# Kernel tuning notes

Hardware: AMD Instinct MI355X
Metric: run time of the kernel (lower is better)

Reference implementation:

```python
import jax, jax.numpy as jnp
import numpy as np

N_NODES = 50000
N_EDGES = 800000
DIM = 96
N_LAYERS = 3
N_GRAPHS = 128
OUT_DIM = 10


def setup_inputs() -> dict:
    key = jax.random.key(0)
    ks = jax.random.split(key, 9)
    s = 1.0 / np.sqrt(DIM)
    return {
        "x": jax.random.normal(ks[0], (N_NODES, DIM), dtype=jnp.float32),
        "edge_index": jax.random.randint(ks[1], (2, N_EDGES), 0, N_NODES, dtype=jnp.int32),
        "batch": jnp.sort(jax.random.randint(ks[2], (N_NODES,), 0, N_GRAPHS, dtype=jnp.int32)),
        "W1": jax.random.normal(ks[3], (N_LAYERS, DIM, DIM), dtype=jnp.float32) * s,
        "W2": jax.random.normal(ks[4], (N_LAYERS, DIM, DIM), dtype=jnp.float32) * s,
        "cw1": jax.random.normal(ks[5], (DIM, DIM), dtype=jnp.float32) * s,
        "cb1": jax.random.normal(ks[6], (DIM,), dtype=jnp.float32) * s,
        "cw2": jax.random.normal(ks[7], (DIM, OUT_DIM), dtype=jnp.float32) * s,
        "cb2": jax.random.normal(ks[8], (OUT_DIM,), dtype=jnp.float32) * s,
    }


def reference(x, edge_index, batch, W1, W2, cw1, cb1, cw2, cb2):
    src, dst = edge_index[0], edge_index[1]
    h = x
    for l in range(N_LAYERS):
        self_part = h @ W1[l]                       # [N, D]
        # transform at node level then gather per edge (same math as per-edge W2(x_j))
        msg = (h @ W2[l])[src]                      # [E, D]
        neighbor_part = jax.ops.segment_sum(msg, dst, num_segments=N_NODES)
        h = jax.nn.relu(self_part + neighbor_part)
    graph_emb = jax.ops.segment_sum(h, batch, num_segments=N_GRAPHS)  # [G, D]
    hidden = jax.nn.relu(graph_emb @ cw1 + cb1)
    return hidden @ cw2 + cb2                       # [G, OUT_DIM]
```

## Files before the change

kernel.cpp:

```cpp
#include <hip/hip_runtime.h>

#define N_NODES   50000
#define N_EDGES   800000
#define DIM       96
#define N_GRAPHS  128
#define OUT_DIM   10
#define NPAD      50048
#define CAP       64
#define NBINS     391
#define BINCAP    4096
#define P1_BLOCKS 256
#define EPB       (N_EDGES / P1_BLOCKS)
#define LPAD      104

#define CAST_NB   ((N_NODES * 12 + 255) / 256)
#define CONV_NB   ((3 * DIM * 2 * DIM + 255) / 256)
#define ZERO_NB   ((NBINS * 16 + 255) / 256)

typedef __attribute__((ext_vector_type(8))) short          short8;
typedef __attribute__((ext_vector_type(8))) unsigned short u16x8;
typedef __attribute__((ext_vector_type(4))) float          f32x4;

__device__ __forceinline__ float b2f(unsigned short u) {
    union { unsigned int i; float f; } v; v.i = ((unsigned int)u) << 16; return v.f;
}
__device__ __forceinline__ unsigned short f2b(float f) {
    union { float f; unsigned int i; } v; v.f = f;
    unsigned int u = v.i;
    return (unsigned short)((u + 0x7fffu + ((u >> 16) & 1u)) >> 16);
}

__global__ __launch_bounds__(256) void prep(const float* __restrict__ x,
                                            const float* __restrict__ W1,
                                            const float* __restrict__ W2,
                                            unsigned short* __restrict__ harr,
                                            unsigned short* __restrict__ Bt,
                                            int* __restrict__ gcur)
{
    const int b = blockIdx.x;
    const int t = threadIdx.x;
    if (b < CAST_NB) {
        const int tid = b * 256 + t;
        if (tid >= N_NODES * 12) return;
        const int node = tid / 12;
        const int c    = (tid - node * 12) * 8;
        const float4 v0 = *(const float4*)(x + (size_t)node * DIM + c);
        const float4 v1 = *(const float4*)(x + (size_t)node * DIM + c + 4);
        u16x8 o;
        o[0] = f2b(v0.x); o[1] = f2b(v0.y); o[2] = f2b(v0.z); o[3] = f2b(v0.w);
        o[4] = f2b(v1.x); o[5] = f2b(v1.y); o[6] = f2b(v1.z); o[7] = f2b(v1.w);
        *(u16x8*)(harr + (size_t)node * DIM + c) = o;
    } else if (b < CAST_NB + CONV_NB) {
        const int idx = (b - CAST_NB) * 256 + t;
        if (idx >= 3 * DIM * 2 * DIM) return;
        const int l   = idx / (DIM * 2 * DIM);
        const int rem = idx - l * (DIM * 2 * DIM);
        const int n   = rem / (2 * DIM);
        const int k   = rem - n * (2 * DIM);
        const float v = (k < DIM) ? W1[(size_t)l * DIM * DIM + k * DIM + n]
                                  : W2[(size_t)l * DIM * DIM + (k - DIM) * DIM + n];
        Bt[idx] = f2b(v);
    } else {
        const int i = (b - CAST_NB - CONV_NB) * 256 + t;
        if (i < NBINS * 16) gcur[i] = 0;
    }
}

__global__ __launch_bounds__(256) void pass1_bin(const int* __restrict__ src,
                                                 const int* __restrict__ dst,
                                                 int* __restrict__ gcur,
                                                 int* __restrict__ binned)
{
    __shared__ int hist[NBINS];
    __shared__ int base[NBINS];
    const int t  = threadIdx.x;
    const int e0 = blockIdx.x * EPB;

    for (int b = t; b < NBINS; b += 256) hist[b] = 0;
    __syncthreads();

    for (int e = e0 + t; e < e0 + EPB; e += 256)
        atomicAdd(&hist[dst[e] >> 7], 1);
    __syncthreads();

    for (int b = t; b < NBINS; b += 256) {
        const int c = hist[b];
        base[b] = (c > 0) ? atomicAdd(&gcur[b << 4], c) : 0;
        hist[b] = 0;
    }
    __syncthreads();

    for (int e = e0 + t; e < e0 + EPB; e += 256) {
        const int d   = dst[e];
        const int bin = d >> 7;
        const int pos = base[bin] + atomicAdd(&hist[bin], 1);
        if (pos < BINCAP)
            binned[bin * BINCAP + pos] = ((d & 127) << 16) | src[e];
    }
}

__global__ __launch_bounds__(256) void pass2_scatter(const int* __restrict__ gcur,
                                                     const int* __restrict__ binned,
                                                     int* __restrict__ csrc,
                                                     int* __restrict__ deg)
{
    __shared__ int ncnt[128];
    const int bin = blockIdx.x;
    const int t   = threadIdx.x;
    const int n0  = bin << 7;
    const int cnt = min(gcur[bin << 4], BINCAP);

    if (t < 128) ncnt[t] = 0;
    __syncthreads();

    const int* __restrict__ bb = binned + bin * BINCAP;
    for (int i = t; i < cnt; i += 256) {
        const int v    = bb[i];
        const int dlow = v >> 16;
        const int s    = v & 0xffff;
        const int pos  = atomicAdd(&ncnt[dlow], 1);
        if (pos < CAP) csrc[(size_t)(n0 + dlow) * CAP + pos] = s;
    }
    __syncthreads();

    if (t < 128 && n0 + t < N_NODES) deg[n0 + t] = min(ncnt[t], CAP);
}

__global__ __launch_bounds__(384) void gnn_layer(
    const unsigned short* __restrict__ harr, const int* __restrict__ deg,
    const int* __restrict__ csrc, const unsigned short* __restrict__ Btl,
    unsigned short* __restrict__ hout)
{
    __shared__ unsigned short aggLds[64][LPAD];
    const int t       = threadIdx.x;
    const int rowBase = blockIdx.x * 64;

    {
        const int r    = t / 6;
        const int sub  = t - r * 6;
        const int node = rowBase + r;
        const int off  = sub * 16;

        float a[16];
#pragma unroll
        for (int i = 0; i < 16; i++) a[i] = 0.f;

        if (node < N_NODES) {
            const int d = deg[node];
            const int* __restrict__ bkt = csrc + (size_t)node * CAP;
            const unsigned short* __restrict__ hb = harr + off;

            const int nfull = d & ~3;
            int c = 0;
            for (; c < nfull; c += 4) {
                const int4 s = *(const int4*)(bkt + c);
                const unsigned short* p0 = hb + (size_t)s.x * DIM;
                const unsigned short* p1 = hb + (size_t)s.y * DIM;
                const unsigned short* p2 = hb + (size_t)s.z * DIM;
                const unsigned short* p3 = hb + (size_t)s.w * DIM;
                const u16x8 va0 = *(const u16x8*)(p0), vb0 = *(const u16x8*)(p0 + 8);
                const u16x8 va1 = *(const u16x8*)(p1), vb1 = *(const u16x8*)(p1 + 8);
                const u16x8 va2 = *(const u16x8*)(p2), vb2 = *(const u16x8*)(p2 + 8);
                const u16x8 va3 = *(const u16x8*)(p3), vb3 = *(const u16x8*)(p3 + 8);
#pragma unroll
                for (int i = 0; i < 8; i++) {
                    a[i]     += b2f(va0[i]) + b2f(va1[i]) + b2f(va2[i]) + b2f(va3[i]);
                    a[i + 8] += b2f(vb0[i]) + b2f(vb1[i]) + b2f(vb2[i]) + b2f(vb3[i]);
                }
            }
            for (; c < d; c++) {
                const unsigned short* p0 = hb + (size_t)bkt[c] * DIM;
                const u16x8 va0 = *(const u16x8*)(p0), vb0 = *(const u16x8*)(p0 + 8);
#pragma unroll
                for (int i = 0; i < 8; i++) {
                    a[i]     += b2f(va0[i]);
                    a[i + 8] += b2f(vb0[i]);
                }
            }
        }

        u16x8 o0, o1;
#pragma unroll
        for (int i = 0; i < 8; i++) { o0[i] = f2b(a[i]); o1[i] = f2b(a[i + 8]); }
        *(u16x8*)(&aggLds[r][off])     = o0;
        *(u16x8*)(&aggLds[r][off + 8]) = o1;
    }
    __syncthreads();

    const int lane = t & 63;
    const int w    = t >> 6;
    const int m    = lane & 15;
    const int q    = lane >> 4;

    short8 bfrag[6];
#pragma unroll
    for (int s = 0; s < 6; s++)
        bfrag[s] = *(const short8*)(Btl + (size_t)(w * 16 + m) * (2 * DIM) + s * 32 + q * 8);

#pragma unroll
    for (int r = 0; r < 4; r++) {
        const int rb = rowBase + r * 16;
        f32x4 acc = {0.f, 0.f, 0.f, 0.f};
        const unsigned short* ah = harr + (size_t)(rb + m) * DIM + q * 8;
#pragma unroll
        for (int s = 0; s < 3; s++) {
            const short8 af = *(const short8*)(ah + s * 32);
            acc = __builtin_amdgcn_mfma_f32_16x16x32_bf16(af, bfrag[s], acc, 0, 0, 0);
        }
#pragma unroll
        for (int s = 0; s < 3; s++) {
            const short8 af = *(const short8*)(&aggLds[r * 16 + m][s * 32 + q * 8]);
            acc = __builtin_amdgcn_mfma_f32_16x16x32_bf16(af, bfrag[s + 3], acc, 0, 0, 0);
        }
#pragma unroll
        for (int i = 0; i < 4; i++) {
            const int grow = rb + q * 4 + i;
            if (grow < N_NODES)
                hout[(size_t)grow * DIM + w * 16 + m] = f2b(fmaxf(acc[i], 0.f));
        }
    }
}

__global__ __launch_bounds__(384) void pool_classify(
    const unsigned short* __restrict__ h, const int* __restrict__ batch,
    const float* __restrict__ cw1, const float* __restrict__ cb1,
    const float* __restrict__ cw2, const float* __restrict__ cb2,
    float* __restrict__ out)
{
    const int g = blockIdx.x;
    const int t = threadIdx.x;

    int lo = 0, hi = N_NODES;
    while (lo < hi) { int m = (lo + hi) >> 1; if (batch[m] < g) lo = m + 1; else hi = m; }
    const int start = lo;
    hi = N_NODES;
    while (lo < hi) { int m = (lo + hi) >> 1; if (batch[m] < g + 1) lo = m + 1; else hi = m; }
    const int end = lo;

    __shared__ float part[4][DIM];
    __shared__ float gr[DIM];
    __shared__ float hid[DIM];

    const int col = t % DIM;
    const int ty  = t / DIM;

    float s = 0.f;
    for (int n = start + ty; n < end; n += 4)
        s += b2f(h[(size_t)n * DIM + col]);
    part[ty][col] = s;
    __syncthreads();
    if (ty == 0)
        gr[col] = part[0][col] + part[1][col] + part[2][col] + part[3][col];
    __syncthreads();

    float hsum = 0.f;
    const int k0 = ty * (DIM / 4);
#pragma unroll 4
    for (int k = k0; k < k0 + DIM / 4; k++)
        hsum += gr[k] * cw1[k * DIM + col];
    part[ty][col] = hsum;
    __syncthreads();
    if (ty == 0)
        hid[col] = fmaxf(part[0][col] + part[1][col] + part[2][col] + part[3][col]
                         + cb1[col], 0.f);
    __syncthreads();

    if (t < OUT_DIM) {
        float o = cb2[t];
#pragma unroll 4
        for (int k = 0; k < DIM; k++) o += hid[k] * cw2[k * OUT_DIM + t];
        out[g * OUT_DIM + t] = o;
    }
}

extern "C" void kernel_launch(void* const* d_in, const int* in_sizes, int n_in,
                              void* d_out, int out_size, void* d_ws, size_t ws_size,
                              hipStream_t stream)
{
    const float* x     = (const float*)d_in[0];
    const int*   ei    = (const int*)  d_in[1];
    const int*   batch = (const int*)  d_in[2];
    const float* W1    = (const float*)d_in[3];
    const float* W2    = (const float*)d_in[4];
    const float* cw1   = (const float*)d_in[5];
    const float* cb1   = (const float*)d_in[6];
    const float* cw2   = (const float*)d_in[7];
    const float* cb2   = (const float*)d_in[8];
    float*       out   = (float*)d_out;

    const int* src = ei;
    const int* dst = ei + N_EDGES;

    unsigned short* bufA = (unsigned short*)d_ws;
    unsigned short* bufB = bufA + (size_t)NPAD * DIM;
    unsigned short* Bt   = bufB + (size_t)NPAD * DIM;
    int*   gcur   = (int*)(Bt + 3 * DIM * 2 * DIM);
    int*   binned = gcur + NBINS * 16;
    int*   csrc   = binned + (size_t)NBINS * BINCAP;
    int*   deg    = csrc + (size_t)N_NODES * CAP;

    prep<<<CAST_NB + CONV_NB + ZERO_NB, 256, 0, stream>>>(x, W1, W2, bufA, Bt, gcur);
    pass1_bin<<<P1_BLOCKS, 256, 0, stream>>>(src, dst, gcur, binned);
    pass2_scatter<<<NBINS, 256, 0, stream>>>(gcur, binned, csrc, deg);

    unsigned short* hin  = bufA;
    unsigned short* hout = bufB;
    for (int l = 0; l < 3; l++) {
        gnn_layer<<<NPAD / 64, 384, 0, stream>>>(hin, deg, csrc,
                                                 Bt + (size_t)l * DIM * 2 * DIM, hout);
        unsigned short* tmp = hin; hin = hout; hout = tmp;
    }

    pool_classify<<<N_GRAPHS, 384, 0, stream>>>(hin, batch, cw1, cb1, cw2, cb2, out);
}
```

Before: 267.7 us.

## Reorder nodes by in-degree buckets for load-balanced gnn_layer blocks

Nodes are grouped by degree through a counting bucket sort in pass2_scatter, and a new bucket_prefix kernel computes the bucket offsets. Each gnn_layer block then processes 64 nodes of similar degree, found by binary search over those offsets, instead of 64 consecutive nodes. This aims to cut wavefront divergence and tail imbalance in the gather loop. In exchange it adds a small kernel launch, a per-row binary search and indirection, and the A-tile loads and output stores become scattered rows instead of contiguous ones.

```diff
diff --git a/kernel.cpp b/kernel.cpp
--- a/kernel.cpp
+++ b/kernel.cpp
@@ -12,10 +12,13 @@
 #define P1_BLOCKS 256
 #define EPB       (N_EDGES / P1_BLOCKS)
 #define LPAD      104
+#define NDB       65
+#define PBCAP     8192
 
 #define CAST_NB   ((N_NODES * 12 + 255) / 256)
 #define CONV_NB   ((3 * DIM * 2 * DIM + 255) / 256)
-#define ZERO_NB   ((NBINS * 16 + 255) / 256)
+#define ZERO_CNT  ((NBINS + NDB) * 16)
+#define ZERO_NB   ((ZERO_CNT + 255) / 256)
 
 typedef __attribute__((ext_vector_type(8))) short          short8;
 typedef __attribute__((ext_vector_type(8))) unsigned short u16x8;
@@ -62,7 +65,7 @@
         Bt[idx] = f2b(v);
     } else {
         const int i = (b - CAST_NB - CONV_NB) * 256 + t;
-        if (i < NBINS * 16) gcur[i] = 0;
+        if (i < ZERO_CNT) gcur[i] = 0;
     }
 }
 
@@ -102,7 +105,9 @@
 __global__ __launch_bounds__(256) void pass2_scatter(const int* __restrict__ gcur,
                                                      const int* __restrict__ binned,
                                                      int* __restrict__ csrc,
-                                                     int* __restrict__ deg)
+                                                     int* __restrict__ deg,
+                                                     int* __restrict__ bcnt,
+                                                     int* __restrict__ pbin)
 {
     __shared__ int ncnt[128];
     const int bin = blockIdx.x;
@@ -123,29 +128,64 @@
     }
     __syncthreads();
 
-    if (t < 128 && n0 + t < N_NODES) deg[n0 + t] = min(ncnt[t], CAP);
+    if (t < 128 && n0 + t < N_NODES) {
+        const int n = n0 + t;
+        const int d = min(ncnt[t], CAP);
+        deg[n] = d;
+        const int pos = atomicAdd(&bcnt[d << 4], 1);
+        if (pos < PBCAP) pbin[d * PBCAP + pos] = n;
+    }
+}
+
+__global__ __launch_bounds__(128) void bucket_prefix(const int* __restrict__ bcnt,
+                                                     int* __restrict__ boff)
+{
+    __shared__ int c[NDB];
+    const int t = threadIdx.x;
+    if (t < NDB) c[t] = min(bcnt[t << 4], PBCAP);
+    __syncthreads();
+    if (t == 0) {
+        int acc = 0;
+        for (int b = 0; b < NDB; b++) { boff[b] = acc; acc += c[b]; }
+        boff[NDB] = acc;
+    }
 }
 
 __global__ __launch_bounds__(384) void gnn_layer(
     const unsigned short* __restrict__ harr, const int* __restrict__ deg,
-    const int* __restrict__ csrc, const unsigned short* __restrict__ Btl,
+    const int* __restrict__ csrc, const int* __restrict__ pbin,
+    const int* __restrict__ boff, const unsigned short* __restrict__ Btl,
     unsigned short* __restrict__ hout)
 {
     __shared__ unsigned short aggLds[64][LPAD];
+    __shared__ int boffL[NDB + 1];
+    __shared__ int nodeIds[64];
     const int t       = threadIdx.x;
     const int rowBase = blockIdx.x * 64;
 
+    if (t < NDB + 1) boffL[t] = boff[t];
+    __syncthreads();
+
     {
-        const int r    = t / 6;
-        const int sub  = t - r * 6;
-        const int node = rowBase + r;
-        const int off  = sub * 16;
+        const int r   = t / 6;
+        const int sub = t - r * 6;
+        const int g   = rowBase + r;
+        const int off = sub * 16;
+
+        int node = -1;
+        if (g < N_NODES) {
+            int lo = 0, hi = NDB - 1;
+            while (lo < hi) { int mid = (lo + hi + 1) >> 1;
+                              if (boffL[mid] <= g) lo = mid; else hi = mid - 1; }
+            node = pbin[lo * PBCAP + (g - boffL[lo])];
+        }
+        if (sub == 0) nodeIds[r] = node;
 
         float a[16];
 #pragma unroll
         for (int i = 0; i < 16; i++) a[i] = 0.f;
 
-        if (node < N_NODES) {
+        if (node >= 0) {
             const int d = deg[node];
             const int* __restrict__ bkt = csrc + (size_t)node * CAP;
             const unsigned short* __restrict__ hb = harr + off;
@@ -199,9 +239,9 @@
 
 #pragma unroll
     for (int r = 0; r < 4; r++) {
-        const int rb = rowBase + r * 16;
         f32x4 acc = {0.f, 0.f, 0.f, 0.f};
-        const unsigned short* ah = harr + (size_t)(rb + m) * DIM + q * 8;
+        const int nodeA = nodeIds[r * 16 + m];
+        const unsigned short* ah = harr + (size_t)max(nodeA, 0) * DIM + q * 8;
 #pragma unroll
         for (int s = 0; s < 3; s++) {
             const short8 af = *(const short8*)(ah + s * 32);
@@ -214,9 +254,9 @@
         }
 #pragma unroll
         for (int i = 0; i < 4; i++) {
-            const int grow = rb + q * 4 + i;
-            if (grow < N_NODES)
-                hout[(size_t)grow * DIM + w * 16 + m] = f2b(fmaxf(acc[i], 0.f));
+            const int nodeC = nodeIds[r * 16 + q * 4 + i];
+            if (nodeC >= 0)
+                hout[(size_t)nodeC * DIM + w * 16 + m] = f2b(fmaxf(acc[i], 0.f));
         }
     }
 }
@@ -295,18 +335,22 @@
     unsigned short* bufB = bufA + (size_t)NPAD * DIM;
     unsigned short* Bt   = bufB + (size_t)NPAD * DIM;
     int*   gcur   = (int*)(Bt + 3 * DIM * 2 * DIM);
-    int*   binned = gcur + NBINS * 16;
+    int*   bcnt   = gcur + NBINS * 16;
+    int*   binned = bcnt + NDB * 16;
     int*   csrc   = binned + (size_t)NBINS * BINCAP;
     int*   deg    = csrc + (size_t)N_NODES * CAP;
+    int*   pbin   = deg + N_NODES;
+    int*   boff   = pbin + NDB * PBCAP;
 
     prep<<<CAST_NB + CONV_NB + ZERO_NB, 256, 0, stream>>>(x, W1, W2, bufA, Bt, gcur);
     pass1_bin<<<P1_BLOCKS, 256, 0, stream>>>(src, dst, gcur, binned);
-    pass2_scatter<<<NBINS, 256, 0, stream>>>(gcur, binned, csrc, deg);
+    pass2_scatter<<<NBINS, 256, 0, stream>>>(gcur, binned, csrc, deg, bcnt, pbin);
+    bucket_prefix<<<1, 128, 0, stream>>>(bcnt, boff);
 
     unsigned short* hin  = bufA;
     unsigned short* hout = bufB;
     for (int l = 0; l < 3; l++) {
-        gnn_layer<<<NPAD / 64, 384, 0, stream>>>(hin, deg, csrc,
+        gnn_layer<<<NPAD / 64, 384, 0, stream>>>(hin, deg, csrc, pbin, boff,
                                                  Bt + (size_t)l * DIM * 2 * DIM, hout);
         unsigned short* tmp = hin; hin = hout; hout = tmp;
     }
```

Result: slower. 361.9 us (+35.2%).

## Replace global-atomic edge binning with per-block slices and prefix scan

Applied to the files above, without the earlier changes.

Edge binning now has each of 128 blocks write into its own fixed-size slice per destination bin. Per-slice counts replace the global atomic cursor and its zeroing pass. The scatter pass prefix-scans the slice counts and binary-searches each edge's slice. This removes one histogram pass and the global atomics, but adds a scan and a binary search per edge in pass 2. The fixed slice capacity of 48 may drop edges if a block holds more than 48 edges for one bin. The layer kernel also issues its weight-fragment loads before the aggregation phase so they can overlap it.

```diff
diff --git a/kernel.cpp b/kernel.cpp
--- a/kernel.cpp
+++ b/kernel.cpp
@@ -6,16 +6,15 @@
 #define N_GRAPHS  128
 #define OUT_DIM   10
 #define NPAD      50048
+#define NBINS     391
+#define P1_BLOCKS 128
+#define EPB       (N_EDGES / P1_BLOCKS)
+#define SLICECAP  48
 #define CAP       64
-#define NBINS     391
-#define BINCAP    4096
-#define P1_BLOCKS 256
-#define EPB       (N_EDGES / P1_BLOCKS)
 #define LPAD      104
 
 #define CAST_NB   ((N_NODES * 12 + 255) / 256)
 #define CONV_NB   ((3 * DIM * 2 * DIM + 255) / 256)
-#define ZERO_NB   ((NBINS * 16 + 255) / 256)
 
 typedef __attribute__((ext_vector_type(8))) short          short8;
 typedef __attribute__((ext_vector_type(8))) unsigned short u16x8;
@@ -34,8 +33,7 @@
                                             const float* __restrict__ W1,
                                             const float* __restrict__ W2,
                                             unsigned short* __restrict__ harr,
-                                            unsigned short* __restrict__ Bt,
-                                            int* __restrict__ gcur)
+                                            unsigned short* __restrict__ Bt)
 {
     const int b = blockIdx.x;
     const int t = threadIdx.x;
@@ -50,7 +48,7 @@
         o[0] = f2b(v0.x); o[1] = f2b(v0.y); o[2] = f2b(v0.z); o[3] = f2b(v0.w);
         o[4] = f2b(v1.x); o[5] = f2b(v1.y); o[6] = f2b(v1.z); o[7] = f2b(v1.w);
         *(u16x8*)(harr + (size_t)node * DIM + c) = o;
-    } else if (b < CAST_NB + CONV_NB) {
+    } else {
         const int idx = (b - CAST_NB) * 256 + t;
         if (idx >= 3 * DIM * 2 * DIM) return;
         const int l   = idx / (DIM * 2 * DIM);
@@ -60,62 +58,71 @@
         const float v = (k < DIM) ? W1[(size_t)l * DIM * DIM + k * DIM + n]
                                   : W2[(size_t)l * DIM * DIM + (k - DIM) * DIM + n];
         Bt[idx] = f2b(v);
-    } else {
-        const int i = (b - CAST_NB - CONV_NB) * 256 + t;
-        if (i < NBINS * 16) gcur[i] = 0;
     }
 }
 
 __global__ __launch_bounds__(256) void pass1_bin(const int* __restrict__ src,
                                                  const int* __restrict__ dst,
-                                                 int* __restrict__ gcur,
-                                                 int* __restrict__ binned)
-{
-    __shared__ int hist[NBINS];
-    __shared__ int base[NBINS];
-    const int t  = threadIdx.x;
-    const int e0 = blockIdx.x * EPB;
-
-    for (int b = t; b < NBINS; b += 256) hist[b] = 0;
-    __syncthreads();
-
-    for (int e = e0 + t; e < e0 + EPB; e += 256)
-        atomicAdd(&hist[dst[e] >> 7], 1);
-    __syncthreads();
-
-    for (int b = t; b < NBINS; b += 256) {
-        const int c = hist[b];
-        base[b] = (c > 0) ? atomicAdd(&gcur[b << 4], c) : 0;
-        hist[b] = 0;
-    }
+                                                 int* __restrict__ binned,
+                                                 int* __restrict__ cnt)
+{
+    __shared__ int cur[NBINS];
+    const int t   = threadIdx.x;
+    const int blk = blockIdx.x;
+    const int e0  = blk * EPB;
+
+    for (int b = t; b < NBINS; b += 256) cur[b] = 0;
     __syncthreads();
 
     for (int e = e0 + t; e < e0 + EPB; e += 256) {
         const int d   = dst[e];
         const int bin = d >> 7;
-        const int pos = base[bin] + atomicAdd(&hist[bin], 1);
-        if (pos < BINCAP)
-            binned[bin * BINCAP + pos] = ((d & 127) << 16) | src[e];
-    }
-}
-
-__global__ __launch_bounds__(256) void pass2_scatter(const int* __restrict__ gcur,
+        const int pos = atomicAdd(&cur[bin], 1);
+        if (pos < SLICECAP)
+            binned[((size_t)bin * P1_BLOCKS + blk) * SLICECAP + pos]
+                = ((d & 127) << 16) | src[e];
+    }
+    __syncthreads();
+
+    for (int b = t; b < NBINS; b += 256)
+        cnt[b * P1_BLOCKS + blk] = min(cur[b], SLICECAP);
+}
+
+__global__ __launch_bounds__(256) void pass2_scatter(const int* __restrict__ cnt,
                                                      const int* __restrict__ binned,
                                                      int* __restrict__ csrc,
                                                      int* __restrict__ deg)
 {
+    __shared__ int buf[2][P1_BLOCKS];
+    __shared__ int soff[P1_BLOCKS + 1];
     __shared__ int ncnt[128];
     const int bin = blockIdx.x;
     const int t   = threadIdx.x;
     const int n0  = bin << 7;
-    const int cnt = min(gcur[bin << 4], BINCAP);
-
-    if (t < 128) ncnt[t] = 0;
-    __syncthreads();
-
-    const int* __restrict__ bb = binned + bin * BINCAP;
-    for (int i = t; i < cnt; i += 256) {
-        const int v    = bb[i];
+
+    if (t < P1_BLOCKS) { buf[0][t] = cnt[bin * P1_BLOCKS + t]; ncnt[t] = 0; }
+    __syncthreads();
+
+    int c = 0;
+#pragma unroll
+    for (int off = 1; off < P1_BLOCKS; off <<= 1) {
+        if (t < P1_BLOCKS) {
+            int x = buf[c][t];
+            if (t >= off) x += buf[c][t - off];
+            buf[c ^ 1][t] = x;
+        }
+        __syncthreads();
+        c ^= 1;
+    }
+    if (t < P1_BLOCKS) { soff[t + 1] = buf[c][t]; if (t == 0) soff[0] = 0; }
+    __syncthreads();
+
+    const int Eb = soff[P1_BLOCKS];
+    for (int i = t; i < Eb; i += 256) {
+        int lo = 0, hi = P1_BLOCKS - 1;
+        while (lo < hi) { int mid = (lo + hi + 1) >> 1;
+                          if (soff[mid] <= i) lo = mid; else hi = mid - 1; }
+        const int v    = binned[((size_t)bin * P1_BLOCKS + lo) * SLICECAP + (i - soff[lo])];
         const int dlow = v >> 16;
         const int s    = v & 0xffff;
         const int pos  = atomicAdd(&ncnt[dlow], 1);
@@ -134,6 +141,15 @@
     __shared__ unsigned short aggLds[64][LPAD];
     const int t       = threadIdx.x;
     const int rowBase = blockIdx.x * 64;
+
+    const int lane = t & 63;
+    const int w    = t >> 6;
+    const int m    = lane & 15;
+    const int q    = lane >> 4;
+    short8 bfrag[6];
+#pragma unroll
+    for (int s = 0; s < 6; s++)
+        bfrag[s] = *(const short8*)(Btl + (size_t)(w * 16 + m) * (2 * DIM) + s * 32 + q * 8);
 
     {
         const int r    = t / 6;
@@ -187,16 +203,6 @@
     }
     __syncthreads();
 
-    const int lane = t & 63;
-    const int w    = t >> 6;
-    const int m    = lane & 15;
-    const int q    = lane >> 4;
-
-    short8 bfrag[6];
-#pragma unroll
-    for (int s = 0; s < 6; s++)
-        bfrag[s] = *(const short8*)(Btl + (size_t)(w * 16 + m) * (2 * DIM) + s * 32 + q * 8);
-
 #pragma unroll
     for (int r = 0; r < 4; r++) {
         const int rb = rowBase + r * 16;
@@ -294,14 +300,14 @@
     unsigned short* bufA = (unsigned short*)d_ws;
     unsigned short* bufB = bufA + (size_t)NPAD * DIM;
     unsigned short* Bt   = bufB + (size_t)NPAD * DIM;
-    int*   gcur   = (int*)(Bt + 3 * DIM * 2 * DIM);
-    int*   binned = gcur + NBINS * 16;
-    int*   csrc   = binned + (size_t)NBINS * BINCAP;
+    int*   cnt    = (int*)(Bt + 3 * DIM * 2 * DIM);
+    int*   binned = cnt + NBINS * P1_BLOCKS;
+    int*   csrc   = binned + (size_t)NBINS * P1_BLOCKS * SLICECAP;
     int*   deg    = csrc + (size_t)N_NODES * CAP;
 
-    prep<<<CAST_NB + CONV_NB + ZERO_NB, 256, 0, stream>>>(x, W1, W2, bufA, Bt, gcur);
-    pass1_bin<<<P1_BLOCKS, 256, 0, stream>>>(src, dst, gcur, binned);
-    pass2_scatter<<<NBINS, 256, 0, stream>>>(gcur, binned, csrc, deg);
+    prep<<<CAST_NB + CONV_NB, 256, 0, stream>>>(x, W1, W2, bufA, Bt);
+    pass1_bin<<<P1_BLOCKS, 256, 0, stream>>>(src, dst, binned, cnt);
+    pass2_scatter<<<NBINS, 256, 0, stream>>>(cnt, binned, csrc, deg);
 
     unsigned short* hin  = bufA;
     unsigned short* hout = bufB;
```

Measured after the change: 275.9 us. 3.1% more time.
